# Performance work log

Hardware: AMD Instinct MI355X
Metric: run time of the kernel (lower is better)

The kernel has to match this reference:

```python
import jax, jax.numpy as jnp
import numpy as np

MARGIN = 0.3
BIG = 1e6  # matches the 1000000.0 additive mask in the torch code


def setup_inputs() -> dict:
    key = jax.random.key(0)
    k1, k2 = jax.random.split(key)
    embeddings = jax.random.normal(k1, (4096, 512), dtype=jnp.float32)
    labels = jax.random.randint(k2, (4096,), 0, 512)
    return {"embeddings": embeddings, "labels": labels}


def reference(embeddings, labels):
    # Pairwise euclidean distances (torch.cdist p=2) via the GEMM identity,
    # clamped before sqrt for numerical safety on the zero diagonal.
    sq = jnp.sum(embeddings * embeddings, axis=1)                      # [N]
    d2 = sq[:, None] + sq[None, :] - 2.0 * (embeddings @ embeddings.T)  # [N, N]
    dist = jnp.sqrt(jnp.maximum(d2, 1e-12))

    pos_mask = labels[None, :] == labels[:, None]   # [N, N] bool
    neg_mask = ~pos_mask

    # Hardest positive per anchor (self-distance 0 is harmless under max).
    hp = jnp.max(dist * pos_mask.astype(dist.dtype), axis=1)           # [N]

    # Semi-hard negatives: hp < d(a, n) < hp + margin, different label.
    semi_hard = (dist > hp[:, None]) & (dist < hp[:, None] + MARGIN) & neg_mask
    has_semi_hard = jnp.sum(semi_hard) > 0

    # Fallback: hardest (farthest) negative; semi-hard branch: closest semi-hard.
    hn_fallback = jnp.max(dist * neg_mask.astype(dist.dtype), axis=1)
    hn_semi = jnp.min(dist + (1.0 - semi_hard.astype(dist.dtype)) * BIG, axis=1)
    hn = jnp.where(has_semi_hard, hn_semi, hn_fallback)                # [N]

    triplet = jax.nn.relu(hp - hn + MARGIN)                            # [N]
    num_valid = jnp.sum((triplet > 0).astype(triplet.dtype))
    loss = jnp.where(num_valid > 0,
                     jnp.sum(triplet) / jnp.maximum(num_valid, 1.0),
                     jnp.mean(triplet))
    return loss
```

## Files before the change

kernel.cpp:

```cpp
#include <hip/hip_runtime.h>
#include <math.h>


constexpr float MARGIN = 0.3f;

typedef _Float16 half8    __attribute__((ext_vector_type(8)));
typedef float    floatx16 __attribute__((ext_vector_type(16)));

#define GLD_LDS16(gp, lp)                                                              \
    __builtin_amdgcn_global_load_lds(                                                  \
        (const __attribute__((address_space(1))) void*)(gp),                           \
        (__attribute__((address_space(3))) void*)(lp), 16, 0, 0)

__global__ __launch_bounds__(256)
void prep_kernel(const float* __restrict__ e, _Float16* __restrict__ pan,
                 float* __restrict__ sq, unsigned int* __restrict__ hp,
                 unsigned int* __restrict__ hn_fall, unsigned int* __restrict__ hn_semi,
                 unsigned int* __restrict__ bars, int N, int D) {
    __shared__ float red[256];
    if (blockIdx.x == 0 && threadIdx.x < 32) bars[threadIdx.x * 32] = 0u;
    const int r0  = blockIdx.x * 8;
    const int p   = r0 >> 7;
    const int rl  = r0 & 127;
    const int r   = threadIdx.x & 7;
    const int c8  = threadIdx.x >> 3;
    const int row = r0 + r;
    const float* er = e + (size_t)row * D;
    float s = 0.f;
    #pragma unroll
    for (int it = 0; it < 2; ++it) {
        const int kw = c8 + it * 32;
        const float4 x0 = *(const float4*)&er[kw * 8];
        const float4 x1 = *(const float4*)&er[kw * 8 + 4];
        const float xv[8] = {x0.x, x0.y, x0.z, x0.w, x1.x, x1.y, x1.z, x1.w};
        half8 hi, lo;
        #pragma unroll
        for (int jj = 0; jj < 8; ++jj) {
            _Float16 h = (_Float16)xv[jj];
            hi[jj] = h;
            lo[jj] = (_Float16)(xv[jj] - (float)h);
            s += xv[jj] * xv[jj];
        }
        *(half8*)&pan[((size_t)(p * 128 + kw) * 128 + rl + r) * 8]      = hi;
        *(half8*)&pan[((size_t)(p * 128 + 64 + kw) * 128 + rl + r) * 8] = lo;
    }
    red[threadIdx.x] = s;
    __syncthreads();
    if (threadIdx.x < 8) {
        float t = 0.f;
        #pragma unroll
        for (int c = 0; c < 32; ++c) t += red[threadIdx.x + 8 * c];
        const int rw = r0 + threadIdx.x;
        sq[rw]      = t;
        hp[rw]      = 0u;
        hn_fall[rw] = 0u;
        hn_semi[rw] = 0x7f800000u;
    }
}

__global__ __launch_bounds__(512, 2)
void fused_kernel(const _Float16* __restrict__ pan, const int* __restrict__ labels,
                  const float* __restrict__ sq,
                  unsigned int* __restrict__ hp,
                  unsigned int* __restrict__ hn_fall,
                  unsigned int* __restrict__ hn_semi,
                  unsigned int* __restrict__ bars,
                  float* __restrict__ out,
                  int N, int D, unsigned int nrowblocks, unsigned int nblocks) {
    __shared__ __attribute__((aligned(16))) _Float16 S[2][32768];
    __shared__ float sq_r[256], sq_c[256], hp_r[256];
    __shared__ int   lab_r[256], lab_c[256];
    __shared__ int   lastflag;

    const int tid  = threadIdx.x;
    const int lane = tid & 63;
    const int wave = tid >> 6;
    const int wr   = (wave >> 2) * 128;
    const int wcol = (wave & 3) * 64;
    const int mrow = lane & 31;
    const int half_id = lane >> 5;

    const int j  = blockIdx.x & 7;
    const int i  = blockIdx.x >> 3;
    const int px = (j & 3) * 4 + (i & 3);
    const int py = (j >> 2) * 8 + (i >> 2);
    const int rowBase = py * 256;
    const int colBase = px * 256;

    if (tid < 256) {
        sq_r[tid]  = sq[rowBase + tid];
        lab_r[tid] = labels[rowBase + tid];
    } else {
        const int t2 = tid - 256;
        sq_c[t2]  = sq[colBase + t2];
        lab_c[t2] = labels[colBase + t2];
    }

    floatx16 acc[2][4];
    #pragma unroll
    for (int b = 0; b < 2; ++b)
        #pragma unroll
        for (int a = 0; a < 4; ++a)
            #pragma unroll
            for (int r = 0; r < 16; ++r) acc[b][a][r] = 0.f;

    auto stage_slab = [&](int buf, int t, int u) {
        const int s = wave * 8 + u;
        int kcl, pp, rowin, lofs;
        if (s < 32) {
            kcl = s >> 2; const int rq = s & 3;
            pp    = 2 * py + (rq >> 1);
            rowin = (rq & 1) * 64 + lane;
            lofs  = (kcl * 256 + rq * 64) * 8;
        } else {
            const int u2 = s - 32;
            kcl = u2 >> 2; const int cq = u2 & 3;
            pp    = 2 * px + (cq >> 1);
            rowin = (cq & 1) * 64 + lane;
            lofs  = 16384 + (kcl * 256 + cq * 64) * 8;
        }
        const int kc = (kcl < 4) ? (4 * t + kcl) : (64 + 4 * t + (kcl - 4));
        const _Float16* g = pan + ((size_t)(pp * 128 + kc) * 128 + rowin) * 8;
        GLD_LDS16(g, &S[buf][lofs]);
    };

    #pragma unroll
    for (int u = 0; u < 8; ++u) stage_slab(0, 0, u);
    __syncthreads();

    #pragma unroll 1
    for (int t = 0; t < 16; ++t) {
        const int cur = t & 1;
        const _Float16* Sc = &S[cur][0];
        if (t + 1 < 16) {
            #pragma unroll
            for (int u = 0; u < 8; ++u) stage_slab(cur ^ 1, t + 1, u);
        }
        auto mm = [&](const half8* bq, const half8* aq) {
            #pragma unroll
            for (int bj = 0; bj < 2; ++bj)
                #pragma unroll
                for (int ai = 0; ai < 4; ++ai)
                    acc[bj][ai] = __builtin_amdgcn_mfma_f32_32x32x16_f16(
                        bq[bj], aq[ai], acc[bj][ai], 0, 0, 0);
        };
        #pragma unroll
        for (int ks = 0; ks < 2; ++ks) {
            const int kb = 2 * ks;
            half8 ah[4], bh[2], al[4], bl[2];
            #pragma unroll
            for (int ai = 0; ai < 4; ++ai)
                ah[ai] = *(const half8*)&Sc[((kb + half_id) * 256 + wr + ai * 32 + mrow) * 8];
            #pragma unroll
            for (int bj = 0; bj < 2; ++bj)
                bh[bj] = *(const half8*)&Sc[16384 + ((kb + half_id) * 256 + wcol + bj * 32 + mrow) * 8];
            #pragma unroll
            for (int ai = 0; ai < 4; ++ai)
                al[ai] = *(const half8*)&Sc[((4 + kb + half_id) * 256 + wr + ai * 32 + mrow) * 8];
            #pragma unroll
            for (int bj = 0; bj < 2; ++bj)
                bl[bj] = *(const half8*)&Sc[16384 + ((4 + kb + half_id) * 256 + wcol + bj * 32 + mrow) * 8];
            __builtin_amdgcn_s_setprio(1);
            mm(bh, ah);
            mm(bh, al);
            mm(bl, ah);
            __builtin_amdgcn_s_setprio(0);
        }
        asm volatile("s_waitcnt vmcnt(0)" ::: "memory");
        __builtin_amdgcn_s_barrier();
        asm volatile("" ::: "memory");
    }

    float sqr[4]; int labr[4];
    #pragma unroll
    for (int ai = 0; ai < 4; ++ai) {
        sqr[ai]  = sq_r[wr + ai * 32 + mrow];
        labr[ai] = lab_r[wr + ai * 32 + mrow];
    }

    #pragma unroll
    for (int ai = 0; ai < 4; ++ai) {
        float vp = 0.f, vn = 0.f;
        #pragma unroll
        for (int bj = 0; bj < 2; ++bj) {
            #pragma unroll
            for (int r = 0; r < 16; ++r) {
                const int c = wcol + bj * 32 + (r & 3) + 8 * (r >> 2) + 4 * half_id;
                float d = sqrtf(fmaxf(sqr[ai] + sq_c[c] - 2.0f * acc[bj][ai][r], 1e-12f));
                const bool pos = (labr[ai] == lab_c[c]);
                vp = fmaxf(vp, pos ? d : 0.f);
                vn = fmaxf(vn, pos ? 0.f : d);
            }
        }
        vp = fmaxf(vp, __shfl_xor(vp, 32, 64));
        vn = fmaxf(vn, __shfl_xor(vn, 32, 64));
        if (half_id == 0) {
            atomicMax(&hp[rowBase + wr + ai * 32 + mrow],      __float_as_uint(vp));
            atomicMax(&hn_fall[rowBase + wr + ai * 32 + mrow], __float_as_uint(vn));
        }
    }

    __syncthreads();
    unsigned int* ctr = &bars[py * 32];
    if (tid == 0) {
        __threadfence();
        atomicAdd(ctr, 1u);
        while (__hip_atomic_load(ctr, __ATOMIC_ACQUIRE, __HIP_MEMORY_SCOPE_AGENT)
               < nrowblocks)
            __builtin_amdgcn_s_sleep(32);
    }
    __syncthreads();
    if (tid < 256)
        hp_r[tid] = __uint_as_float(__hip_atomic_load(&hp[rowBase + tid],
                                    __ATOMIC_RELAXED, __HIP_MEMORY_SCOPE_AGENT));
    __syncthreads();

    #pragma unroll
    for (int ai = 0; ai < 4; ++ai) {
        const float hpv = hp_r[wr + ai * 32 + mrow];
        float vm = __builtin_inff();
        #pragma unroll
        for (int bj = 0; bj < 2; ++bj) {
            #pragma unroll
            for (int r = 0; r < 16; ++r) {
                const int c = wcol + bj * 32 + (r & 3) + 8 * (r >> 2) + 4 * half_id;
                float d = sqrtf(fmaxf(sqr[ai] + sq_c[c] - 2.0f * acc[bj][ai][r], 1e-12f));
                const bool cand = (labr[ai] != lab_c[c]) && (d > hpv);
                vm = fminf(vm, cand ? d : __builtin_inff());
            }
        }
        vm = fminf(vm, __shfl_xor(vm, 32, 64));
        if (half_id == 0)
            atomicMin(&hn_semi[rowBase + wr + ai * 32 + mrow], __float_as_uint(vm));
    }

    __syncthreads();
    if (tid == 0) {
        __threadfence();
        unsigned int old = atomicAdd(&bars[992], 1u);
        lastflag = (old == nblocks - 1) ? 1 : 0;
    }
    __syncthreads();
    if (!lastflag) return;
    if (tid == 0) __threadfence();
    __syncthreads();

    float* FS = (float*)&S[0][0];
    int*   IC = (int*)(FS + 512);
    int*   IA = IC + 512;
    int any = 0;
    for (int r = tid; r < N; r += 512) {
        float h  = __uint_as_float(__hip_atomic_load(&hp[r],      __ATOMIC_RELAXED, __HIP_MEMORY_SCOPE_AGENT));
        float hs = __uint_as_float(__hip_atomic_load(&hn_semi[r], __ATOMIC_RELAXED, __HIP_MEMORY_SCOPE_AGENT));
        any |= (hs < h + MARGIN) ? 1 : 0;
    }
    IA[tid] = any;
    __syncthreads();
    for (int s = 256; s; s >>= 1) {
        if (tid < s) IA[tid] |= IA[tid + s];
        __syncthreads();
    }
    const bool has_semi = IA[0] != 0;
    float sum = 0.f; int valid = 0;
    for (int r = tid; r < N; r += 512) {
        float h  = __uint_as_float(__hip_atomic_load(&hp[r], __ATOMIC_RELAXED, __HIP_MEMORY_SCOPE_AGENT));
        float hn = has_semi
            ? __uint_as_float(__hip_atomic_load(&hn_semi[r], __ATOMIC_RELAXED, __HIP_MEMORY_SCOPE_AGENT))
            : __uint_as_float(__hip_atomic_load(&hn_fall[r], __ATOMIC_RELAXED, __HIP_MEMORY_SCOPE_AGENT));
        float t = fmaxf(h - hn + MARGIN, 0.f);
        if (!(t > 0.f)) t = 0.f;
        sum += t;
        valid += (t > 0.f) ? 1 : 0;
    }
    FS[tid] = sum; IC[tid] = valid;
    __syncthreads();
    for (int s = 256; s; s >>= 1) {
        if (tid < s) { FS[tid] += FS[tid + s]; IC[tid] += IC[tid + s]; }
        __syncthreads();
    }
    if (tid == 0) {
        float total = FS[0]; int v = IC[0];
        out[0] = (v > 0) ? (total / (float)v) : (total / (float)N);
    }
}

extern "C" void kernel_launch(void* const* d_in, const int* in_sizes, int n_in,
                              void* d_out, int out_size, void* d_ws, size_t ws_size,
                              hipStream_t stream) {
    const float* e      = (const float*)d_in[0];
    const int*   labels = (const int*)d_in[1];
    const int N = in_sizes[1];
    const int D = in_sizes[0] / N;
    float* out = (float*)d_out;

    float*        sq      = (float*)d_ws;
    unsigned int* hp      = (unsigned int*)d_ws + N;
    unsigned int* hn_fall = hp + N;
    unsigned int* hn_semi = hn_fall + N;
    unsigned int* bars    = hn_semi + N;

    const size_t small_bytes = ((size_t)(4 * N + 1024) * 4 + 255) & ~(size_t)255;
    _Float16* pan = (_Float16*)((char*)d_ws + small_bytes);

    prep_kernel<<<N / 8, 256, 0, stream>>>(e, pan, sq, hp, hn_fall, hn_semi, bars, N, D);

    const int ntx = N / 256, nty = N / 256;
    fused_kernel<<<ntx * nty, 512, 0, stream>>>(pan, labels, sq, hp, hn_fall, hn_semi,
                                                bars, out, N, D,
                                                (unsigned)ntx, (unsigned)(ntx * nty));
}
```

Before: 137.5 us.

## Fold prep pass into fused kernel behind a grid-wide barrier

The separate prep kernel, which converts embeddings to split hi/lo fp16 panels and computes row norms, now runs at the start of the fused kernel. Each of the 256 blocks handles 16 rows, then all blocks wait on a global atomic barrier before the GEMM phase. Barrier counters are zeroed with a memset instead of inside prep. This removes one kernel launch and its tail, but adds a memset, a grid-wide spin barrier, and lowers the occupancy hint from 2 to 1 block per CU. The barrier relies on all 256 blocks being resident at once.

New measurement: 151.8 us. 10.4% more time.

```diff
diff --git a/kernel.cpp b/kernel.cpp
--- a/kernel.cpp
+++ b/kernel.cpp
@@ -12,55 +12,9 @@
         (const __attribute__((address_space(1))) void*)(gp),                           \
         (__attribute__((address_space(3))) void*)(lp), 16, 0, 0)
 
-__global__ __launch_bounds__(256)
-void prep_kernel(const float* __restrict__ e, _Float16* __restrict__ pan,
-                 float* __restrict__ sq, unsigned int* __restrict__ hp,
-                 unsigned int* __restrict__ hn_fall, unsigned int* __restrict__ hn_semi,
-                 unsigned int* __restrict__ bars, int N, int D) {
-    __shared__ float red[256];
-    if (blockIdx.x == 0 && threadIdx.x < 32) bars[threadIdx.x * 32] = 0u;
-    const int r0  = blockIdx.x * 8;
-    const int p   = r0 >> 7;
-    const int rl  = r0 & 127;
-    const int r   = threadIdx.x & 7;
-    const int c8  = threadIdx.x >> 3;
-    const int row = r0 + r;
-    const float* er = e + (size_t)row * D;
-    float s = 0.f;
-    #pragma unroll
-    for (int it = 0; it < 2; ++it) {
-        const int kw = c8 + it * 32;
-        const float4 x0 = *(const float4*)&er[kw * 8];
-        const float4 x1 = *(const float4*)&er[kw * 8 + 4];
-        const float xv[8] = {x0.x, x0.y, x0.z, x0.w, x1.x, x1.y, x1.z, x1.w};
-        half8 hi, lo;
-        #pragma unroll
-        for (int jj = 0; jj < 8; ++jj) {
-            _Float16 h = (_Float16)xv[jj];
-            hi[jj] = h;
-            lo[jj] = (_Float16)(xv[jj] - (float)h);
-            s += xv[jj] * xv[jj];
-        }
-        *(half8*)&pan[((size_t)(p * 128 + kw) * 128 + rl + r) * 8]      = hi;
-        *(half8*)&pan[((size_t)(p * 128 + 64 + kw) * 128 + rl + r) * 8] = lo;
-    }
-    red[threadIdx.x] = s;
-    __syncthreads();
-    if (threadIdx.x < 8) {
-        float t = 0.f;
-        #pragma unroll
-        for (int c = 0; c < 32; ++c) t += red[threadIdx.x + 8 * c];
-        const int rw = r0 + threadIdx.x;
-        sq[rw]      = t;
-        hp[rw]      = 0u;
-        hn_fall[rw] = 0u;
-        hn_semi[rw] = 0x7f800000u;
-    }
-}
-
-__global__ __launch_bounds__(512, 2)
-void fused_kernel(const _Float16* __restrict__ pan, const int* __restrict__ labels,
-                  const float* __restrict__ sq,
+__global__ __launch_bounds__(512, 1)
+void fused_kernel(const float* __restrict__ e, const int* __restrict__ labels,
+                  _Float16* __restrict__ pan, float* __restrict__ sq,
                   unsigned int* __restrict__ hp,
                   unsigned int* __restrict__ hn_fall,
                   unsigned int* __restrict__ hn_semi,
@@ -68,11 +22,63 @@
                   float* __restrict__ out,
                   int N, int D, unsigned int nrowblocks, unsigned int nblocks) {
     __shared__ __attribute__((aligned(16))) _Float16 S[2][32768];
+    __shared__ float red[512];
     __shared__ float sq_r[256], sq_c[256], hp_r[256];
     __shared__ int   lab_r[256], lab_c[256];
     __shared__ int   lastflag;
 
     const int tid  = threadIdx.x;
+
+    {
+        const int r0  = blockIdx.x * 16;
+        const int p   = r0 >> 7;
+        const int rl  = r0 & 127;
+        const int rr  = tid & 15;
+        const int c8  = tid >> 4;
+        const int row = r0 + rr;
+        const float* er = e + (size_t)row * D;
+        float s = 0.f;
+        #pragma unroll
+        for (int it = 0; it < 2; ++it) {
+            const int kw = c8 + it * 32;
+            const float4 x0 = *(const float4*)&er[kw * 8];
+            const float4 x1 = *(const float4*)&er[kw * 8 + 4];
+            const float xv[8] = {x0.x, x0.y, x0.z, x0.w, x1.x, x1.y, x1.z, x1.w};
+            half8 hi, lo;
+            #pragma unroll
+            for (int jj = 0; jj < 8; ++jj) {
+                _Float16 h = (_Float16)xv[jj];
+                hi[jj] = h;
+                lo[jj] = (_Float16)(xv[jj] - (float)h);
+                s += xv[jj] * xv[jj];
+            }
+            *(half8*)&pan[((size_t)(p * 128 + kw) * 128 + rl + rr) * 8]      = hi;
+            *(half8*)&pan[((size_t)(p * 128 + 64 + kw) * 128 + rl + rr) * 8] = lo;
+        }
+        red[tid] = s;
+        __syncthreads();
+        if (tid < 16) {
+            float t = 0.f;
+            #pragma unroll
+            for (int c = 0; c < 32; ++c) t += red[tid + 16 * c];
+            const int rw = r0 + tid;
+            sq[rw]      = t;
+            hp[rw]      = 0u;
+            hn_fall[rw] = 0u;
+            hn_semi[rw] = 0x7f800000u;
+        }
+    }
+
+    __syncthreads();
+    if (tid == 0) {
+        __threadfence();
+        atomicAdd(&bars[0], 1u);
+        while (__hip_atomic_load(&bars[0], __ATOMIC_ACQUIRE,
+                                 __HIP_MEMORY_SCOPE_AGENT) < nblocks)
+            __builtin_amdgcn_s_sleep(32);
+    }
+    __syncthreads();
+
     const int lane = tid & 63;
     const int wave = tid >> 6;
     const int wr   = (wave >> 2) * 128;
@@ -201,7 +207,7 @@
     }
 
     __syncthreads();
-    unsigned int* ctr = &bars[py * 32];
+    unsigned int* ctr = &bars[32 + py * 32];
     if (tid == 0) {
         __threadfence();
         atomicAdd(ctr, 1u);
@@ -299,13 +305,13 @@
     unsigned int* hn_semi = hn_fall + N;
     unsigned int* bars    = hn_semi + N;
 
-    const size_t small_bytes = ((size_t)(4 * N + 1024) * 4 + 255) & ~(size_t)255;
+    const size_t small_bytes = ((size_t)(4 * N + 2048) * 4 + 255) & ~(size_t)255;
     _Float16* pan = (_Float16*)((char*)d_ws + small_bytes);
 
-    prep_kernel<<<N / 8, 256, 0, stream>>>(e, pan, sq, hp, hn_fall, hn_semi, bars, N, D);
+    hipMemsetAsync(bars, 0, 2048 * sizeof(unsigned int), stream);
 
     const int ntx = N / 256, nty = N / 256;
-    fused_kernel<<<ntx * nty, 512, 0, stream>>>(pan, labels, sq, hp, hn_fall, hn_semi,
-                                                bars, out, N, D,
+    fused_kernel<<<ntx * nty, 512, 0, stream>>>(e, labels, pan, sq, hp, hn_fall,
+                                                hn_semi, bars, out, N, D,
                                                 (unsigned)ntx, (unsigned)(ntx * nty));
 }
```
